# Optimization experiments

Hardware: AMD Instinct MI355X
Metric: run time of the kernel (lower is better)

The kernel has to match this reference:

```python
import jax, jax.numpy as jnp
import numpy as np

I = 512
H = 512
B = 64
T = 512

def _lstm_step(W_ih, W_hh, b_ih, b_hh):
    def step(carry, xt):
        h, c = carry
        # gates in torch LSTMCell order: i, f, g, o
        gates = xt @ W_ih.T + b_ih + h @ W_hh.T + b_hh  # [B, 4H]
        i, f, g, o = jnp.split(gates, 4, axis=-1)
        c = jax.nn.sigmoid(f) * c + jax.nn.sigmoid(i) * jnp.tanh(g)
        h = jax.nn.sigmoid(o) * jnp.tanh(c)
        return (h, c), h
    return step

def setup_inputs() -> dict:
    key = jax.random.key(0)
    ks = jax.random.split(key, 9)
    s = 1.0 / np.sqrt(H)  # torch LSTMCell init: U(-1/sqrt(H), 1/sqrt(H))
    u = lambda k, shp: jax.random.uniform(k, shp, jnp.float32, -s, s)
    return {
        "xs": jax.random.normal(ks[0], (B, T, I), jnp.float32),
        "W_ih_f": u(ks[1], (4 * H, I)), "W_hh_f": u(ks[2], (4 * H, H)),
        "b_ih_f": u(ks[3], (4 * H,)), "b_hh_f": u(ks[4], (4 * H,)),
        "W_ih_b": u(ks[5], (4 * H, I)), "W_hh_b": u(ks[6], (4 * H, H)),
        "b_ih_b": u(ks[7], (4 * H,)), "b_hh_b": u(ks[8], (4 * H,)),
    }

def reference(xs, W_ih_f, W_hh_f, b_ih_f, b_hh_f, W_ih_b, W_hh_b, b_ih_b, b_hh_b):
    x = jnp.transpose(xs, (1, 0, 2))  # batch_first -> [T, B, I]
    b, h = x.shape[1], W_hh_f.shape[1]
    init = (jnp.zeros((b, h), x.dtype), jnp.zeros((b, h), x.dtype))
    _, hs_fwd = jax.lax.scan(_lstm_step(W_ih_f, W_hh_f, b_ih_f, b_hh_f), init, x)
    # reverse direction: scan backward, outputs land at original time indices
    _, hs_bwd = jax.lax.scan(_lstm_step(W_ih_b, W_hh_b, b_ih_b, b_hh_b), init, x, reverse=True)
    rst = jnp.concatenate([hs_fwd, hs_bwd], axis=-1)  # [T, B, 2H]
    return jnp.transpose(rst, (1, 0, 2))  # back to [B, T, 2H]
```

## Files before the change

### kernel.cpp

```cpp
#include <hip/hip_runtime.h>
#include <math.h>

#define B 64
#define T 512
#define II 512
#define H 512
#define NBLK 256

typedef float f32x4 __attribute__((ext_vector_type(4)));
typedef short s16x8 __attribute__((ext_vector_type(8)));
typedef unsigned u32;
typedef unsigned long long u64;

union pk8 { s16x8 v; u32 u[4]; };

__device__ __forceinline__ unsigned short f2b(float f){
  union { float f; u32 u; } v; v.f = f;
  u32 r = v.u + 0x7fffu + ((v.u >> 16) & 1u);
  return (unsigned short)(r >> 16);
}

__device__ __forceinline__ s16x8 cvt8(float4 lo, float4 hi){
  pk8 r;
  asm("v_cvt_pk_bf16_f32 %0, %1, %2" : "=v"(r.u[0]) : "v"(lo.x), "v"(lo.y));
  asm("v_cvt_pk_bf16_f32 %0, %1, %2" : "=v"(r.u[1]) : "v"(lo.z), "v"(lo.w));
  asm("v_cvt_pk_bf16_f32 %0, %1, %2" : "=v"(r.u[2]) : "v"(hi.x), "v"(hi.y));
  asm("v_cvt_pk_bf16_f32 %0, %1, %2" : "=v"(r.u[3]) : "v"(hi.z), "v"(hi.w));
  return r.v;
}

__device__ __forceinline__ float sigm_(float x){
  return __builtin_amdgcn_rcpf(1.f + __expf(-x));
}
__device__ __forceinline__ float tanh_(float x){
  float t = __expf(-2.f * fabsf(x));
  float r = (1.f - t) * __builtin_amdgcn_rcpf(1.f + t);
  return copysignf(r, x);
}

__device__ __forceinline__ u32 ld_sc0_u32(const u32* p){
  u32 v;
  asm volatile("global_load_dword %0, %1, off sc0\n\ts_waitcnt vmcnt(0)"
               : "=v"(v) : "v"(p) : "memory");
  return v;
}
__device__ __forceinline__ void st_sc0_u32(u32* p, u32 v){
  asm volatile("global_store_dword %0, %1, off sc0" : : "v"(p), "v"(v) : "memory");
}
__device__ __forceinline__ void ld4_sc0_issue(const void* p0, const void* p1,
                                              const void* p2, const void* p3,
                                              uint4& a, uint4& b, uint4& c, uint4& d){
  asm volatile(
    "global_load_dwordx4 %0, %4, off sc0\n\t"
    "global_load_dwordx4 %1, %5, off sc0\n\t"
    "global_load_dwordx4 %2, %6, off sc0\n\t"
    "global_load_dwordx4 %3, %7, off sc0"
    : "=&v"(a), "=&v"(b), "=&v"(c), "=&v"(d)
    : "v"(p0), "v"(p1), "v"(p2), "v"(p3)
    : "memory");
}

__global__ void init_ws(u32* p, int n){
  int i = blockIdx.x*blockDim.x + threadIdx.x;
  for (; i < n; i += gridDim.x*blockDim.x)
    __hip_atomic_store(p + i, 0u, __ATOMIC_RELAXED, __HIP_MEMORY_SCOPE_AGENT);
}

__global__ __launch_bounds__(256, 1) void lstm_persistent(
    const float* __restrict__ xs,
    const float* __restrict__ Wih_f, const float* __restrict__ Whh_f,
    const float* __restrict__ bih_f, const float* __restrict__ bhh_f,
    const float* __restrict__ Wih_b, const float* __restrict__ Whh_b,
    const float* __restrict__ bih_b, const float* __restrict__ bhh_b,
    float* __restrict__ out,
    u32* __restrict__ flags,
    u32* __restrict__ roster,
    u32* __restrict__ hbuf0, u32* __restrict__ hbuf1)
{
  __shared__ unsigned short Wlds[4*16*1024];
  __shared__ unsigned short Hlds[16*512];
  __shared__ float g_lds[4][16][16];
  __shared__ float bias_s[64];
  __shared__ u32 role_s;

  const int tid = threadIdx.x;

  if (tid == 0){
    u32 xcc;
    asm volatile("s_getreg_b32 %0, hwreg(HW_REG_XCC_ID, 0, 32)" : "=s"(xcc));
    xcc &= 7u;
    u32 slot = __hip_atomic_fetch_add(&roster[xcc], 1u,
                                      __ATOMIC_RELAXED, __HIP_MEMORY_SCOPE_AGENT);
    role_s = (xcc << 5) | (slot & 31u);
  }
  __syncthreads();
  const u32 role = role_s;
  const int grp   = role >> 5;
  const int qtile = role & 31;
  const int dir   = grp >> 2;
  const int btile = grp & 3;
  const int q0 = qtile * 16;
  const int b0 = btile * 16;

  const float* __restrict__ Wih = dir ? Wih_b : Wih_f;
  const float* __restrict__ Whh = dir ? Whh_b : Whh_f;
  const float* __restrict__ bih = dir ? bih_b : bih_f;
  const float* __restrict__ bhh = dir ? bhh_b : bhh_f;

  for (int it = 0; it < 32; ++it){
    int idx = it * 256 + tid;
    int c64 = idx >> 7;
    int k   = (idx & 127) * 8;
    int cg  = (c64 >> 4) * H + q0 + (c64 & 15);
    const float* src = (k < II) ? (Wih + (size_t)cg * II + k)
                                : (Whh + (size_t)cg * H + (k - II));
    float4 lo = *(const float4*)src;
    float4 hi = *(const float4*)(src + 4);
    s16x8 v;
    v[0]=(short)f2b(lo.x); v[1]=(short)f2b(lo.y); v[2]=(short)f2b(lo.z); v[3]=(short)f2b(lo.w);
    v[4]=(short)f2b(hi.x); v[5]=(short)f2b(hi.y); v[6]=(short)f2b(hi.z); v[7]=(short)f2b(hi.w);
    u32 byte = ((u32)c64 * 2048u + (u32)k * 2u) ^ (((u32)(c64 & 7)) << 4);
    *(s16x8*)((char*)Wlds + byte) = v;
  }
  if (tid < 64){
    int g = tid >> 4, jj = tid & 15;
    int cg = g * H + q0 + jj;
    bias_s[tid] = bih[cg] + bhh[cg];
  }
  __syncthreads();

  const int w = tid >> 6;
  const int l = tid & 63;
  const int arow = b0 + (l & 15);
  const int kgrp = (l >> 4) * 8;
  const int c64w = (w << 4) | (l & 15);
  const u32 swz   = ((u32)(c64w & 7)) << 4;
  const u32 wbase = (u32)c64w * 2048u;
  const u32 hrb = (u32)(l & 15) * 1024u;
  const u32 hsz = ((u32)(l & 7)) << 4;

  const int sr = w * 4;
  const int si = l;

  const int eb = tid >> 4;
  const int ej = tid & 15;
  float c_reg = 0.f;

  const size_t hdir = (size_t)dir * (B * (H/2));
  u32* const fl = flags + grp * 32;

  s16x8 a_x[16];
  {
    const int t0 = dir ? (T-1) : 0;
    const float* xrow = xs + ((size_t)arow * T + t0) * II + kgrp;
    #pragma unroll
    for (int ks = 0; ks < 16; ++ks)
      a_x[ks] = cvt8(*(const float4*)(xrow + ks*32), *(const float4*)(xrow + ks*32 + 4));
  }

  #pragma unroll 1
  for (int s = 0; s < T; ++s){
    const int t = dir ? (T - 1 - s) : s;
    const u32* __restrict__ hin  = (s & 1) ? hbuf1 : hbuf0;
    u32* __restrict__       hout = (s & 1) ? hbuf0 : hbuf1;

    if (s > 0){
      const u32* fp = fl + (l & 31);
      for (;;){
        u32 v = ld_sc0_u32(fp);
        if (__all((int)(v >= (u32)s))) break;
        __builtin_amdgcn_s_sleep(1);
      }
    }

    const char* hinb = (const char*)(hin + hdir);
    const char* r0p = hinb + (size_t)(b0 + sr + 0) * 1024 + (size_t)si * 16;
    const char* r1p = r0p + 1024;
    const char* r2p = r0p + 2048;
    const char* r3p = r0p + 3072;
    uint4 hva, hvb, hvc, hvd;
    ld4_sc0_issue(r0p, r1p, r2p, r3p, hva, hvb, hvc, hvd);

    f32x4 acc_xa = {0.f,0.f,0.f,0.f}, acc_xb = {0.f,0.f,0.f,0.f};
    #pragma unroll
    for (int ks = 0; ks < 8; ++ks){
      u32 byte0 = (wbase + (u32)(ks*32 + kgrp) * 2u) ^ swz;
      u32 byte1 = (wbase + (u32)((ks+8)*32 + kgrp) * 2u) ^ swz;
      s16x8 b0f = *(const s16x8*)((const char*)Wlds + byte0);
      s16x8 b1f = *(const s16x8*)((const char*)Wlds + byte1);
      acc_xa = __builtin_amdgcn_mfma_f32_16x16x32_bf16(a_x[ks],   b0f, acc_xa, 0, 0, 0);
      acc_xb = __builtin_amdgcn_mfma_f32_16x16x32_bf16(a_x[ks+8], b1f, acc_xb, 0, 0, 0);
    }

    asm volatile("s_waitcnt vmcnt(0)" ::: "memory");
    __builtin_amdgcn_sched_barrier(0);
    {
      u32 byte0 = ((u32)(sr+0) * 1024u + (u32)si * 16u) ^ (((u32)((sr+0) & 7)) << 4);
      u32 byte1 = ((u32)(sr+1) * 1024u + (u32)si * 16u) ^ (((u32)((sr+1) & 7)) << 4);
      u32 byte2 = ((u32)(sr+2) * 1024u + (u32)si * 16u) ^ (((u32)((sr+2) & 7)) << 4);
      u32 byte3 = ((u32)(sr+3) * 1024u + (u32)si * 16u) ^ (((u32)((sr+3) & 7)) << 4);
      *(uint4*)((char*)Hlds + byte0) = hva;
      *(uint4*)((char*)Hlds + byte1) = hvb;
      *(uint4*)((char*)Hlds + byte2) = hvc;
      *(uint4*)((char*)Hlds + byte3) = hvd;
    }
    __syncthreads();

    f32x4 acc_ha = {0.f,0.f,0.f,0.f}, acc_hb = {0.f,0.f,0.f,0.f};
    #pragma unroll
    for (int ks = 0; ks < 8; ++ks){
      u32 hb0 = (hrb + (u32)(ks*64 + (kgrp*2))) ^ hsz;
      u32 hb1 = (hrb + (u32)((ks+8)*64 + (kgrp*2))) ^ hsz;
      s16x8 a0 = *(const s16x8*)((const char*)Hlds + hb0);
      s16x8 a1 = *(const s16x8*)((const char*)Hlds + hb1);
      u32 byte0 = (wbase + (u32)(II + ks*32 + kgrp) * 2u) ^ swz;
      u32 byte1 = (wbase + (u32)(II + (ks+8)*32 + kgrp) * 2u) ^ swz;
      s16x8 b0f = *(const s16x8*)((const char*)Wlds + byte0);
      s16x8 b1f = *(const s16x8*)((const char*)Wlds + byte1);
      acc_ha = __builtin_amdgcn_mfma_f32_16x16x32_bf16(a0, b0f, acc_ha, 0, 0, 0);
      acc_hb = __builtin_amdgcn_mfma_f32_16x16x32_bf16(a1, b1f, acc_hb, 0, 0, 0);
    }

    #pragma unroll
    for (int r = 0; r < 4; ++r){
      int bl = (l >> 4) * 4 + r;
      g_lds[w][bl][l & 15] = acc_xa[r] + acc_xb[r] + acc_ha[r] + acc_hb[r];
    }
    __syncthreads();

    float hn;
    {
      float gi = g_lds[0][eb][ej] + bias_s[ej];
      float gf = g_lds[1][eb][ej] + bias_s[16 + ej];
      float gg = g_lds[2][eb][ej] + bias_s[32 + ej];
      float go = g_lds[3][eb][ej] + bias_s[48 + ej];
      float si_ = sigm_(gi);
      float sf  = sigm_(gf);
      float tg  = tanh_(gg);
      float so  = sigm_(go);
      c_reg = sf * c_reg + si_ * tg;
      hn = so * tanh_(c_reg);
      u32 hb = (u32)f2b(hn);
      u32 nb = (u32)__shfl_xor((int)hb, 1, 64);
      if (!(tid & 1)){
        u32* p = hout + hdir + (size_t)(b0 + eb) * (H/2) + (size_t)((q0 + ej) >> 1);
        st_sc0_u32(p, hb | (nb << 16));
      }
    }

    asm volatile("s_waitcnt vmcnt(0)" ::: "memory");
    __syncthreads();
    if (tid == 0 && s + 1 < T)
      st_sc0_u32(&fl[qtile], (u32)(s + 1));

    out[((size_t)(b0+eb) * T + t) * (2*H) + (size_t)dir * H + (q0 + ej)] = hn;
    if (s + 1 < T){
      const int tn = dir ? (T - 2 - s) : (s + 1);
      const float* xrow = xs + ((size_t)arow * T + tn) * II + kgrp;
      #pragma unroll
      for (int ks = 0; ks < 16; ++ks)
        a_x[ks] = cvt8(*(const float4*)(xrow + ks*32), *(const float4*)(xrow + ks*32 + 4));
    }
  }
}

extern "C" void kernel_launch(void* const* d_in, const int* in_sizes, int n_in,
                              void* d_out, int out_size, void* d_ws, size_t ws_size,
                              hipStream_t stream)
{
  const float* xs    = (const float*)d_in[0];
  const float* Wih_f = (const float*)d_in[1];
  const float* Whh_f = (const float*)d_in[2];
  const float* bih_f = (const float*)d_in[3];
  const float* bhh_f = (const float*)d_in[4];
  const float* Wih_b = (const float*)d_in[5];
  const float* Whh_b = (const float*)d_in[6];
  const float* bih_b = (const float*)d_in[7];
  const float* bhh_b = (const float*)d_in[8];
  float* out = (float*)d_out;

  char* ws = (char*)d_ws;
  u32* flags  = (u32*)ws;
  u32* roster = (u32*)(ws + 2048);
  u32* hbuf0  = (u32*)(ws + 4096);
  u32* hbuf1  = (u32*)(ws + 4096 + 2*B*(H/2)*4);

  const int init_u32 = (4096 + 2*(2*B*(H/2)*4)) / 4;
  init_ws<<<128, 256, 0, stream>>>((u32*)ws, init_u32);

  lstm_persistent<<<NBLK, 256, 0, stream>>>(
      xs, Wih_f, Whh_f, bih_f, bhh_f,
      Wih_b, Whh_b, bih_b, bhh_b,
      out, flags, roster, hbuf0, hbuf1);
}
```

Measured before the change: 2.616 ms.

## Compute next step's input projection before the flag wait, and poll with one wave

The x·W_ih MFMA product for step s+1 is now computed at the end of step s, after the flag publish and before the next flag wait. The resulting accumulators seed the h·W_hh accumulation, so the critical path after the flag wait only covers the recurrent GEMM. Flag polling is limited to wave 0, with a longer sleep, followed by a block barrier, which cuts global polling traffic. In exchange each step gains an extra __syncthreads, and latency may rise if the longer sleep delays wakeup.

Result: no change. 2.590 ms (-1.0%).

```diff
diff --git a/kernel.cpp b/kernel.cpp
--- a/kernel.cpp
+++ b/kernel.cpp
@@ -149,13 +149,21 @@
   const size_t hdir = (size_t)dir * (B * (H/2));
   u32* const fl = flags + grp * 32;
 
-  s16x8 a_x[16];
+  f32x4 acc_xa_n = {0.f,0.f,0.f,0.f}, acc_xb_n = {0.f,0.f,0.f,0.f};
   {
     const int t0 = dir ? (T-1) : 0;
     const float* xrow = xs + ((size_t)arow * T + t0) * II + kgrp;
     #pragma unroll
-    for (int ks = 0; ks < 16; ++ks)
-      a_x[ks] = cvt8(*(const float4*)(xrow + ks*32), *(const float4*)(xrow + ks*32 + 4));
+    for (int ks = 0; ks < 8; ++ks){
+      s16x8 a0 = cvt8(*(const float4*)(xrow + ks*32),     *(const float4*)(xrow + ks*32 + 4));
+      s16x8 a1 = cvt8(*(const float4*)(xrow + (ks+8)*32), *(const float4*)(xrow + (ks+8)*32 + 4));
+      u32 byte0 = (wbase + (u32)(ks*32 + kgrp) * 2u) ^ swz;
+      u32 byte1 = (wbase + (u32)((ks+8)*32 + kgrp) * 2u) ^ swz;
+      s16x8 b0f = *(const s16x8*)((const char*)Wlds + byte0);
+      s16x8 b1f = *(const s16x8*)((const char*)Wlds + byte1);
+      acc_xa_n = __builtin_amdgcn_mfma_f32_16x16x32_bf16(a0, b0f, acc_xa_n, 0, 0, 0);
+      acc_xb_n = __builtin_amdgcn_mfma_f32_16x16x32_bf16(a1, b1f, acc_xb_n, 0, 0, 0);
+    }
   }
 
   #pragma unroll 1
@@ -165,12 +173,15 @@
     u32* __restrict__       hout = (s & 1) ? hbuf0 : hbuf1;
 
     if (s > 0){
-      const u32* fp = fl + (l & 31);
-      for (;;){
-        u32 v = ld_sc0_u32(fp);
-        if (__all((int)(v >= (u32)s))) break;
-        __builtin_amdgcn_s_sleep(1);
+      if (w == 0){
+        const u32* fp = fl + (l & 31);
+        for (;;){
+          u32 v = ld_sc0_u32(fp);
+          if (__all((int)(v >= (u32)s))) break;
+          __builtin_amdgcn_s_sleep(2);
+        }
       }
+      __syncthreads();
     }
 
     const char* hinb = (const char*)(hin + hdir);
@@ -180,18 +191,6 @@
     const char* r3p = r0p + 3072;
     uint4 hva, hvb, hvc, hvd;
     ld4_sc0_issue(r0p, r1p, r2p, r3p, hva, hvb, hvc, hvd);
-
-    f32x4 acc_xa = {0.f,0.f,0.f,0.f}, acc_xb = {0.f,0.f,0.f,0.f};
-    #pragma unroll
-    for (int ks = 0; ks < 8; ++ks){
-      u32 byte0 = (wbase + (u32)(ks*32 + kgrp) * 2u) ^ swz;
-      u32 byte1 = (wbase + (u32)((ks+8)*32 + kgrp) * 2u) ^ swz;
-      s16x8 b0f = *(const s16x8*)((const char*)Wlds + byte0);
-      s16x8 b1f = *(const s16x8*)((const char*)Wlds + byte1);
-      acc_xa = __builtin_amdgcn_mfma_f32_16x16x32_bf16(a_x[ks],   b0f, acc_xa, 0, 0, 0);
-      acc_xb = __builtin_amdgcn_mfma_f32_16x16x32_bf16(a_x[ks+8], b1f, acc_xb, 0, 0, 0);
-    }
-
     asm volatile("s_waitcnt vmcnt(0)" ::: "memory");
     __builtin_amdgcn_sched_barrier(0);
     {
@@ -206,7 +205,7 @@
     }
     __syncthreads();
 
-    f32x4 acc_ha = {0.f,0.f,0.f,0.f}, acc_hb = {0.f,0.f,0.f,0.f};
+    f32x4 acc_ha = acc_xa_n, acc_hb = acc_xb_n;
     #pragma unroll
     for (int ks = 0; ks < 8; ++ks){
       u32 hb0 = (hrb + (u32)(ks*64 + (kgrp*2))) ^ hsz;
@@ -224,7 +223,7 @@
     #pragma unroll
     for (int r = 0; r < 4; ++r){
       int bl = (l >> 4) * 4 + r;
-      g_lds[w][bl][l & 15] = acc_xa[r] + acc_xb[r] + acc_ha[r] + acc_hb[r];
+      g_lds[w][bl][l & 15] = acc_ha[r] + acc_hb[r];
     }
     __syncthreads();
 
@@ -257,9 +256,20 @@
     if (s + 1 < T){
       const int tn = dir ? (T - 2 - s) : (s + 1);
       const float* xrow = xs + ((size_t)arow * T + tn) * II + kgrp;
+      f32x4 na = {0.f,0.f,0.f,0.f}, nb2 = {0.f,0.f,0.f,0.f};
       #pragma unroll
-      for (int ks = 0; ks < 16; ++ks)
-        a_x[ks] = cvt8(*(const float4*)(xrow + ks*32), *(const float4*)(xrow + ks*32 + 4));
+      for (int ks = 0; ks < 8; ++ks){
+        s16x8 a0 = cvt8(*(const float4*)(xrow + ks*32),     *(const float4*)(xrow + ks*32 + 4));
+        s16x8 a1 = cvt8(*(const float4*)(xrow + (ks+8)*32), *(const float4*)(xrow + (ks+8)*32 + 4));
+        u32 byte0 = (wbase + (u32)(ks*32 + kgrp) * 2u) ^ swz;
+        u32 byte1 = (wbase + (u32)((ks+8)*32 + kgrp) * 2u) ^ swz;
+        s16x8 b0f = *(const s16x8*)((const char*)Wlds + byte0);
+        s16x8 b1f = *(const s16x8*)((const char*)Wlds + byte1);
+        na  = __builtin_amdgcn_mfma_f32_16x16x32_bf16(a0, b0f, na,  0, 0, 0);
+        nb2 = __builtin_amdgcn_mfma_f32_16x16x32_bf16(a1, b1f, nb2, 0, 0, 0);
+      }
+      acc_xa_n = na;
+      acc_xb_n = nb2;
     }
   }
 }
```
